# Optimization experiments

Measured on AMD Instinct MI355X. Metric: run time of the kernel, lower is better.

Reference implementation:

```python
import jax, jax.numpy as jnp
import numpy as np

N_NODES = 50000
N_EDGES = 800000
D = 128        # input_dim == output_dim
D_EDGE = 64    # edge_attr_size
Z_DIM = 2 * D + D_EDGE  # 320


def setup_inputs() -> dict:
    key = jax.random.key(0)
    k1, k2, k3, k4, k5 = jax.random.split(key, 5)
    x = jax.random.normal(k1, (N_NODES, D), dtype=jnp.float32)
    edge_index = jax.random.randint(k2, (2, N_EDGES), 0, N_NODES, dtype=jnp.int64)
    edge_attr = jax.random.normal(k3, (N_EDGES, D_EDGE), dtype=jnp.float32)
    scale = 1.0 / np.sqrt(Z_DIM)
    W_f = jax.random.normal(k4, (Z_DIM, D), dtype=jnp.float32) * scale
    W_s = jax.random.normal(k5, (Z_DIM, D), dtype=jnp.float32) * scale
    b_f = jnp.zeros((D,), dtype=jnp.float32)
    b_s = jnp.zeros((D,), dtype=jnp.float32)
    return {"x": x, "edge_index": edge_index, "edge_attr": edge_attr,
            "W_f": W_f, "b_f": b_f, "W_s": W_s, "b_s": b_s}


def reference(x, edge_index, edge_attr, W_f, b_f, W_s, b_s):
    # Dropout(p=0.0) is identity in inference.
    src = edge_index[0]  # j (message source)
    dst = edge_index[1]  # i (message target)
    # z_e = [x_i, x_j, e_ij]  -> [E, 2D + D_edge]
    z = jnp.concatenate([x[dst], x[src], edge_attr], axis=-1)
    # CGConv message: sigmoid(lin_f(z)) * softplus(lin_s(z))
    msg = jax.nn.sigmoid(z @ W_f + b_f) * jax.nn.softplus(z @ W_s + b_s)
    # scatter-add aggregation + residual
    out = jax.ops.segment_sum(msg, dst, num_segments=x.shape[0]) + x
    # use_activation=True -> ReLU
    return jax.nn.relu(out)
```

## Files before the change

kernel.cpp:

```cpp
#include <hip/hip_runtime.h>
#include <hip/hip_bf16.h>

#define E_TOTAL   800000
#define NN        50000
#define DD        128
#define DE        64
#define ZDIM      320
#define MT        64
#define NTPB      4
#define NBS       196

typedef short bf16x8 __attribute__((ext_vector_type(8)));
typedef float f32x4  __attribute__((ext_vector_type(4)));

__device__ __forceinline__ unsigned short f2bf(float f) {
    union { float f; unsigned int u; } v; v.f = f;
    unsigned int u = v.u;
    return (unsigned short)((u + 0x7fffu + ((u >> 16) & 1u)) >> 16);
}

__device__ __forceinline__ float bf2f(unsigned short h) {
    union { unsigned u; float f; } v; v.u = ((unsigned)h) << 16; return v.f;
}

__device__ __forceinline__ unsigned pkbf2(float a, float b) {
    __hip_bfloat162 h = __float22bfloat162_rn(make_float2(a, b));
    unsigned u; __builtin_memcpy(&u, &h, 4); return u;
}

__device__ __forceinline__ uint2 pkbf4(float4 v) {
    uint2 r; r.x = pkbf2(v.x, v.y); r.y = pkbf2(v.z, v.w); return r;
}

__device__ __forceinline__ float fast_rcp(float x) {
#if __has_builtin(__builtin_amdgcn_rcpf)
    return __builtin_amdgcn_rcpf(x);
#else
    return 1.0f / x;
#endif
}

__device__ __forceinline__ void barrier_lgkm() {
    __builtin_amdgcn_sched_barrier(0);
    asm volatile("s_waitcnt lgkmcnt(0)" ::: "memory");
    __builtin_amdgcn_s_barrier();
    __builtin_amdgcn_sched_barrier(0);
}


__global__ void scan_part(const int* __restrict__ counts, int* __restrict__ partial) {
    __shared__ int red[256];
    int t = threadIdx.x, k = blockIdx.x * 256 + t;
    red[t] = (k < NN) ? counts[k] : 0;
    __syncthreads();
    for (int d = 128; d > 0; d >>= 1) {
        if (t < d) red[t] += red[t + d];
        __syncthreads();
    }
    if (t == 0) partial[blockIdx.x] = red[0];
}

__global__ void scan_top(int* __restrict__ partial) {
    __shared__ int s[256];
    int t = threadIdx.x;
    int v = (t < NBS) ? partial[t] : 0;
    s[t] = v; __syncthreads();
    for (int d = 1; d < 256; d <<= 1) {
        int a = (t >= d) ? s[t - d] : 0;
        __syncthreads();
        s[t] += a;
        __syncthreads();
    }
    if (t < NBS) partial[t] = s[t] - v;
}

__global__ void scan_final(const int* __restrict__ counts,
                           const int* __restrict__ partial,
                           int* __restrict__ cursor) {
    __shared__ int s[256];
    int t = threadIdx.x, k = blockIdx.x * 256 + t;
    int v = (k < NN) ? counts[k] : 0;
    s[t] = v; __syncthreads();
    for (int d = 1; d < 256; d <<= 1) {
        int a = (t >= d) ? s[t - d] : 0;
        __syncthreads();
        s[t] += a;
        __syncthreads();
    }
    if (k < NN) cursor[k] = partial[blockIdx.x] + s[t] - v;
}

__global__ void scan_final2(const int* __restrict__ counts,
                            const int* __restrict__ partial,
                            int* __restrict__ cursor) {
    __shared__ int s[256], p2[256], orig[256];
    int t = threadIdx.x, k = blockIdx.x * 256 + t;
    int pv = (t < NBS) ? partial[t] : 0;
    p2[t] = pv; orig[t] = pv; __syncthreads();
    for (int d = 1; d < 256; d <<= 1) {
        int a = (t >= d) ? p2[t - d] : 0;
        __syncthreads();
        p2[t] += a;
        __syncthreads();
    }
    int blkoff = p2[blockIdx.x] - orig[blockIdx.x];
    int v = (k < NN) ? counts[k] : 0;
    s[t] = v; __syncthreads();
    for (int d = 1; d < 256; d <<= 1) {
        int a = (t >= d) ? s[t - d] : 0;
        __syncthreads();
        s[t] += a;
        __syncthreads();
    }
    if (k < NN) cursor[k] = blkoff + s[t] - v;
}

__global__ void scatter_kernel(const int* __restrict__ ei, int* __restrict__ cursor,
                               uint2* __restrict__ spak2) {
    int e = blockIdx.x * 256 + threadIdx.x;
    if (e < E_TOTAL) {
        int d = ei[E_TOTAL + e];
        int pos = atomicAdd(&cursor[d], 1);
        uint2 p; p.x = ((unsigned)d << 16) | (unsigned)ei[e]; p.y = (unsigned)e;
        spak2[pos] = p;
    }
}


__global__ void prep_kernel4(const int* __restrict__ ei,
                             const float* __restrict__ W_f,
                             const float* __restrict__ W_s,
                             unsigned short* __restrict__ WtE,
                             unsigned short* __restrict__ WtN,
                             int* __restrict__ counts,
                             float* __restrict__ aggr) {
    int id = blockIdx.x * 256 + threadIdx.x;
    float4 z; z.x = 0.f; z.y = 0.f; z.z = 0.f; z.w = 0.f;
    ((float4*)aggr)[id] = z;
    if (id < E_TOTAL) atomicAdd(&counts[ei[E_TOTAL + id]], 1);
    if (id < 256 * DE) {
        int n = id >> 6, k = id & 63;
        int ok = 2 * DD + k;
        float wv = (n < DD) ? W_f[ok * DD + n] : W_s[ok * DD + (n - DD)];
        WtE[id] = f2bf(wv);
    } else if (id < 256 * DE + 2 * 256 * DD) {
        int id2 = id - 256 * DE;
        int part = id2 >> 15;
        int r = id2 & 32767;
        int n = r >> 7, k = r & 127;
        int ok = part * DD + k;
        float wv = (n < DD) ? W_f[ok * DD + n] : W_s[ok * DD + (n - DD)];
        WtN[id2] = f2bf(wv);
    }
}

__global__ __launch_bounds__(512, 4)
void node_kernel3(const float* __restrict__ x,
                  const unsigned short* __restrict__ WtN,
                  const float* __restrict__ bf_, const float* __restrict__ bs_,
                  unsigned int* __restrict__ nodeP32) {
    __shared__ unsigned short A_lds[MT * DD];
    const int t = threadIdx.x;
    const int m_off = blockIdx.x * MT;
    const int lane = t & 63, w8 = t >> 6;
    const int part = w8 >> 2, w = w8 & 3;
    const int l15 = lane & 15, quad = lane >> 4;

    #pragma unroll
    for (int it = 0; it < 4; ++it) {
        int idx = it * 512 + t;
        int e = idx >> 5, kq = idx & 31;
        int row = m_off + e; if (row >= NN) row = NN - 1;
        float4 v = ((const float4*)(x + (size_t)row * DD))[kq];
        int g = kq >> 1;
        int col = ((g & ~7) | ((g & 7) ^ (e & 7))) * 8 + (kq & 1) * 4;
        *((uint2*)&A_lds[e * DD + col]) = pkbf4(v);
    }

    f32x4 acc[4][4] = {};
    const int nt0 = 2 * w;
    const unsigned short* Bp[4];
    #pragma unroll
    for (int u = 0; u < 4; ++u) {
        int nt = nt0 + ((u < 2) ? u : (6 + u));
        Bp[u] = WtN + (size_t)part * (256 * DD) +
                (size_t)(nt * 16 + l15) * DD + quad * 8;
    }
    __syncthreads();

    #pragma unroll
    for (int ks = 0; ks < 4; ++ks) {
        bf16x8 af[4], bfr[4];
        #pragma unroll
        for (int i = 0; i < 4; ++i) {
            int m = i * 16 + l15;
            int g = 4 * ks + quad;
            int col = ((g & ~7) | ((g & 7) ^ (l15 & 7))) * 8;
            af[i] = *((const bf16x8*)&A_lds[m * DD + col]);
        }
        #pragma unroll
        for (int u = 0; u < 4; ++u)
            bfr[u] = *((const bf16x8*)(Bp[u] + ks * 32));
        #pragma unroll
        for (int i = 0; i < 4; ++i)
            #pragma unroll
            for (int u = 0; u < 4; ++u)
                acc[i][u] = __builtin_amdgcn_mfma_f32_16x16x32_bf16(
                    af[i], bfr[u], acc[i][u], 0, 0, 0);
    }

    const int c0 = 32 * w + l15, c1 = c0 + 16;
    const float bf0 = part ? 0.f : bf_[c0], bs0 = part ? 0.f : bs_[c0];
    const float bf1 = part ? 0.f : bf_[c1], bs1 = part ? 0.f : bs_[c1];
    #pragma unroll
    for (int i = 0; i < 4; ++i)
        #pragma unroll
        for (int j = 0; j < 4; ++j) {
            int e = i * 16 + quad * 4 + j;
            int row = m_off + e;
            if (row < NN) {
                unsigned int* np = nodeP32 + (size_t)row * 256 + part * 128;
                np[c0] = pkbf2(acc[i][0][j] + bf0, acc[i][2][j] + bs0);
                np[c1] = pkbf2(acc[i][1][j] + bf1, acc[i][3][j] + bs1);
            }
        }
}


#define ISSUE_VA(VA, K)                                                        \
    _Pragma("unroll")                                                          \
    for (int it = 0; it < 2; ++it) {                                           \
        int idx = it * 512 + t;                                                \
        int e = idx >> 4;                                                      \
        VA[it] = ((const float4*)(ea + (size_t)eid_lds[K][e] * DE))[idx & 15]; \
    }

#define ISSUE_GATHER(PS, PD, K)                                                \
    _Pragma("unroll")                                                          \
    for (int i = 0; i < 4; ++i)                                                \
        _Pragma("unroll")                                                      \
        for (int j = 0; j < 4; ++j) {                                          \
            int e = i * 16 + quad * 4 + j;                                     \
            PS[i * 4 + j] = nodeP32[(size_t)src_lds[K][e] * 256 + 128 + c];    \
            PD[i * 4 + j] = nodeP32[(size_t)dst_lds[K][e] * 256 + c];          \
        }

#define STORE_A(VA, BUF)                                                       \
    _Pragma("unroll")                                                          \
    for (int it = 0; it < 2; ++it) {                                           \
        int idx = it * 512 + t;                                                \
        int e = idx >> 4, kq = idx & 15;                                       \
        int colx = (((kq >> 1) & 7) ^ (e & 7)) * 8 + (kq & 1) * 4;             \
        *((uint2*)&A_lds[BUF][e * DE + colx]) = pkbf4(VA[it]);                 \
    }

#define ZERO_ACC                                                               \
    { f32x4 zz = {};                                                           \
      _Pragma("unroll")                                                        \
      for (int i = 0; i < 4; ++i) { acc[i][0] = zz; acc[i][1] = zz; } }

#define GEMM_T(BUF)                                                            \
    _Pragma("unroll")                                                          \
    for (int ks = 0; ks < 2; ++ks) {                                           \
        bf16x8 af[4];                                                          \
        _Pragma("unroll")                                                      \
        for (int i = 0; i < 4; ++i) {                                          \
            int m = i * 16 + l15;                                              \
            int g = 4 * ks + quad;                                             \
            int colx = ((g & 7) ^ (l15 & 7)) * 8;                              \
            af[i] = *((const bf16x8*)&A_lds[BUF][m * DE + colx]);              \
        }                                                                      \
        _Pragma("unroll")                                                      \
        for (int i = 0; i < 4; ++i) {                                          \
            acc[i][0] = __builtin_amdgcn_mfma_f32_16x16x32_bf16(               \
                af[i], bfr[0][ks], acc[i][0], 0, 0, 0);                        \
            acc[i][1] = __builtin_amdgcn_mfma_f32_16x16x32_bf16(               \
                af[i], bfr[1][ks], acc[i][1], 0, 0, 0);                        \
        }                                                                      \
    }

#define EPILOG(PS, PD, K)                                                      \
    {                                                                          \
        int rprev = -1; float s0 = 0.f, nf = 0.f, ns = 0.f;                    \
        _Pragma("unroll")                                                      \
        for (int i = 0; i < 4; ++i)                                            \
            _Pragma("unroll")                                                  \
            for (int j = 0; j < 4; ++j) {                                      \
                int e = i * 16 + quad * 4 + j;                                 \
                int rid = runid_lds[K][e];                                     \
                if (rid != rprev) {                                            \
                    if (rprev >= 0) atomicAdd(&sumb[rprev][c], s0);            \
                    rprev = rid; s0 = 0.f;                                     \
                    unsigned pk = PD[i * 4 + j];                               \
                    nf = bf2f((unsigned short)(pk & 0xffffu));                 \
                    ns = bf2f((unsigned short)(pk >> 16));                     \
                }                                                              \
                unsigned pp = PS[i * 4 + j];                                   \
                float f  = acc[i][0][j] + nf + bf2f((unsigned short)(pp & 0xffffu)); \
                float sg = acc[i][1][j] + ns + bf2f((unsigned short)(pp >> 16));     \
                s0 += fast_rcp(1.f + __expf(-f)) *                             \
                      (fmaxf(sg, 0.f) + __logf(1.f + __expf(-fabsf(sg))));     \
            }                                                                  \
        atomicAdd(&sumb[rprev][c], s0);                                        \
    }

#define WRITEOUT(K)                                                            \
    {                                                                          \
        int ndk = nd_lds[K];                                                   \
        int col = t & 127, rb = t >> 7;                                        \
        for (int r = rb; r < ndk; r += 4) {                                    \
            float v = sumb[r][col];                                            \
            sumb[r][col] = 0.f;                                                \
            float* op = aggr + (size_t)rdst_lds[K][r] * DD + col;              \
            if (rbound_lds[K][r]) atomicAdd(op, v);                            \
            else *op = v;                                                      \
        }                                                                      \
    }

__global__ __launch_bounds__(512, 3)
void edge_kernel4(const float* __restrict__ ea,
                  const unsigned short* __restrict__ WtE,
                  const unsigned int* __restrict__ nodeP32,
                  float* __restrict__ aggr,
                  const uint2* __restrict__ spak2) {
    __shared__ float sumb[MT][DD];
    __shared__ alignas(16) unsigned short A_lds[2][MT * DE];
    __shared__ int dst_lds[NTPB][MT];
    __shared__ int src_lds[NTPB][MT];
    __shared__ int eid_lds[NTPB][MT];
    __shared__ int runid_lds[NTPB][MT];
    __shared__ int rdst_lds[NTPB][MT];
    __shared__ int rbound_lds[NTPB][MT];
    __shared__ int nd_lds[NTPB];

    const int t = threadIdx.x;
    const int blk_e0 = blockIdx.x * (MT * NTPB);
    const int lane = t & 63, w2 = t >> 6, l15 = lane & 15, quad = lane >> 4;
    const int c = 16 * w2 + l15;

    bf16x8 bfr[2][2];
    #pragma unroll
    for (int u = 0; u < 2; ++u) {
        int nt = w2 + u * 8;
        const unsigned short* bp = WtE + (size_t)(nt * 16 + l15) * DE + quad * 8;
        bfr[u][0] = *((const bf16x8*)bp);
        bfr[u][1] = *((const bf16x8*)(bp + 32));
    }

    if (w2 < NTPB) {
        int tb = blk_e0 + w2 * MT;
        uint2 p = spak2[tb + lane];
        int dsv = (int)(p.x >> 16);
        dst_lds[w2][lane] = dsv;
        src_lds[w2][lane] = (int)(p.x & 0xffffu);
        eid_lds[w2][lane] = (int)p.y;
        int updsv = __shfl_up(dsv, 1);
        int flag = (lane == 0 || dsv != updsv) ? 1 : 0;
        unsigned long long m = __ballot(flag != 0);
        int rid = __popcll(m << (63 - lane)) - 1;
        runid_lds[w2][lane] = rid;
        if (flag) { rdst_lds[w2][rid] = dsv; rbound_lds[w2][rid] = 0; }
        int ndv = __popcll(m);
        if (lane == 0) {
            nd_lds[w2] = ndv;
            if (tb > 0 && (int)(spak2[tb - 1].x >> 16) == dsv)
                rbound_lds[w2][0] = 1;
        }
        if (lane == MT - 1) {
            if (tb + MT < E_TOTAL && (int)(spak2[tb + MT].x >> 16) == dsv)
                rbound_lds[w2][ndv - 1] = 1;
        }
    }
    {
        int col = t & 127, rb = t >> 7;
        #pragma unroll
        for (int r = rb; r < MT; r += 4) sumb[r][col] = 0.f;
    }
    __syncthreads();

    float4 vaA[2], vaB[2];
    unsigned psA[16], psB[16], pdA[16], pdB[16];
    f32x4 acc[4][2];

    ISSUE_VA(vaA, 0)
    ISSUE_GATHER(psA, pdA, 0)
    STORE_A(vaA, 0)
    ISSUE_VA(vaB, 1)
    ISSUE_GATHER(psB, pdB, 1)
    barrier_lgkm();

    ZERO_ACC GEMM_T(0)
    EPILOG(psA, pdA, 0)
    ISSUE_VA(vaA, 2)
    ISSUE_GATHER(psA, pdA, 2)
    STORE_A(vaB, 1)
    barrier_lgkm();
    WRITEOUT(0)
    barrier_lgkm();

    ZERO_ACC GEMM_T(1)
    EPILOG(psB, pdB, 1)
    ISSUE_VA(vaB, 3)
    ISSUE_GATHER(psB, pdB, 3)
    STORE_A(vaA, 0)
    barrier_lgkm();
    WRITEOUT(1)
    barrier_lgkm();

    ZERO_ACC GEMM_T(0)
    EPILOG(psA, pdA, 2)
    STORE_A(vaB, 1)
    barrier_lgkm();
    WRITEOUT(2)
    barrier_lgkm();

    ZERO_ACC GEMM_T(1)
    EPILOG(psB, pdB, 3)
    barrier_lgkm();
    WRITEOUT(3)
}

__global__ void relu_kernel4(const float* __restrict__ x,
                             const float* __restrict__ aggr,
                             float* __restrict__ out) {
    int id = blockIdx.x * 256 + threadIdx.x;
    if (id < NN * DD / 4) {
        float4 xv = ((const float4*)x)[id];
        float4 av = ((const float4*)aggr)[id];
        float4 v;
        v.x = fmaxf(xv.x + av.x, 0.0f); v.y = fmaxf(xv.y + av.y, 0.0f);
        v.z = fmaxf(xv.z + av.z, 0.0f); v.w = fmaxf(xv.w + av.w, 0.0f);
        ((float4*)out)[id] = v;
    }
}


__global__ void prep_kernel2(const float* __restrict__ x,
                             const int* __restrict__ ei,
                             const float* __restrict__ W_f,
                             const float* __restrict__ W_s,
                             unsigned short* __restrict__ WtE,
                             unsigned short* __restrict__ WtN,
                             int* __restrict__ counts,
                             float* __restrict__ out) {
    int id = blockIdx.x * 256 + threadIdx.x;
    ((float4*)out)[id] = ((const float4*)x)[id];
    if (id < E_TOTAL) atomicAdd(&counts[ei[E_TOTAL + id]], 1);
    if (id < 256 * DE) {
        int n = id >> 6, k = id & 63;
        int ok = 2 * DD + k;
        float wv = (n < DD) ? W_f[ok * DD + n] : W_s[ok * DD + (n - DD)];
        WtE[id] = f2bf(wv);
    } else if (id < 256 * DE + 2 * 256 * DD) {
        int id2 = id - 256 * DE;
        int part = id2 >> 15;
        int r = id2 & 32767;
        int n = r >> 7, k = r & 127;
        int ok = part * DD + k;
        float wv = (n < DD) ? W_f[ok * DD + n] : W_s[ok * DD + (n - DD)];
        WtN[id2] = f2bf(wv);
    }
}

__global__ __launch_bounds__(256, 4)
void node_kernel2(const float* __restrict__ x,
                  const unsigned short* __restrict__ WtN,
                  const float* __restrict__ bf_, const float* __restrict__ bs_,
                  unsigned int* __restrict__ nodeP32) {
    __shared__ unsigned short A_lds[MT * DD];
    const int t = threadIdx.x;
    const int m_off = blockIdx.x * MT;
    const int part = blockIdx.y;
    const int lane = t & 63, w = t >> 6, l15 = lane & 15, quad = lane >> 4;

    #pragma unroll
    for (int it = 0; it < 8; ++it) {
        int idx = it * 256 + t;
        int e = idx >> 5, kq = idx & 31;
        int row = m_off + e; if (row >= NN) row = NN - 1;
        float4 v = ((const float4*)(x + (size_t)row * DD))[kq];
        int g = kq >> 1;
        int col = ((g & ~7) | ((g & 7) ^ (e & 7))) * 8 + (kq & 1) * 4;
        *((uint2*)&A_lds[e * DD + col]) = pkbf4(v);
    }

    f32x4 acc[4][4] = {};
    const int nt0 = 2 * w;
    const unsigned short* Bp[4];
    #pragma unroll
    for (int u = 0; u < 4; ++u) {
        int nt = nt0 + ((u < 2) ? u : (6 + u));
        Bp[u] = WtN + (size_t)part * (256 * DD) +
                (size_t)(nt * 16 + l15) * DD + quad * 8;
    }
    __syncthreads();

    #pragma unroll
    for (int ks = 0; ks < 4; ++ks) {
        bf16x8 af[4], bfr[4];
        #pragma unroll
        for (int i = 0; i < 4; ++i) {
            int m = i * 16 + l15;
            int g = 4 * ks + quad;
            int col = ((g & ~7) | ((g & 7) ^ (l15 & 7))) * 8;
            af[i] = *((const bf16x8*)&A_lds[m * DD + col]);
        }
        #pragma unroll
        for (int u = 0; u < 4; ++u)
            bfr[u] = *((const bf16x8*)(Bp[u] + ks * 32));
        #pragma unroll
        for (int i = 0; i < 4; ++i)
            #pragma unroll
            for (int u = 0; u < 4; ++u)
                acc[i][u] = __builtin_amdgcn_mfma_f32_16x16x32_bf16(
                    af[i], bfr[u], acc[i][u], 0, 0, 0);
    }

    const int c0 = 32 * w + l15, c1 = c0 + 16;
    const float bf0 = part ? 0.f : bf_[c0], bs0 = part ? 0.f : bs_[c0];
    const float bf1 = part ? 0.f : bf_[c1], bs1 = part ? 0.f : bs_[c1];
    #pragma unroll
    for (int i = 0; i < 4; ++i)
        #pragma unroll
        for (int j = 0; j < 4; ++j) {
            int e = i * 16 + quad * 4 + j;
            int row = m_off + e;
            if (row < NN) {
                unsigned int* np = nodeP32 + (size_t)row * 256 + part * 128;
                np[c0] = pkbf2(acc[i][0][j] + bf0, acc[i][2][j] + bs0);
                np[c1] = pkbf2(acc[i][1][j] + bf1, acc[i][3][j] + bs1);
            }
        }
}

__global__ __launch_bounds__(512, 4)
void edge_kernel2(const float* __restrict__ ea,
                  const unsigned short* __restrict__ WtE,
                  const unsigned int* __restrict__ nodeP32,
                  float* __restrict__ out,
                  const uint2* __restrict__ spak2) {
    __shared__ float sumb[MT][DD];
    __shared__ unsigned short A_lds[MT * DE];
    __shared__ int dst_lds[MT];
    __shared__ int src_lds[MT];
    __shared__ int eid_lds[MT];
    __shared__ int runid_lds[MT];
    __shared__ int rdst_lds[MT];
    __shared__ int rbound_lds[MT];
    __shared__ int ndist_lds;

    const int t = threadIdx.x;
    const int m_off = blockIdx.x * MT;
    const int lane = t & 63, w2 = t >> 6, l15 = lane & 15, quad = lane >> 4;

    if (t < MT) {
        uint2 p = spak2[m_off + t];
        int dsv = (int)(p.x >> 16);
        dst_lds[t] = dsv;
        src_lds[t] = (int)(p.x & 0xffffu);
        eid_lds[t] = (int)p.y;
        int updsv = __shfl_up(dsv, 1);
        int flag = (t == 0 || dsv != updsv) ? 1 : 0;
        unsigned long long m = __ballot(flag != 0);
        int rid = __popcll(m << (63 - t)) - 1;
        runid_lds[t] = rid;
        if (flag) { rdst_lds[rid] = dsv; rbound_lds[rid] = 0; }
        int nd = __popcll(m);
        if (t == 0) {
            ndist_lds = nd;
            if (m_off > 0 && (int)(spak2[m_off - 1].x >> 16) == dsv)
                rbound_lds[0] = 1;
        }
        if (t == MT - 1) {
            if (m_off + MT < E_TOTAL &&
                (int)(spak2[m_off + MT].x >> 16) == dsv)
                rbound_lds[nd - 1] = 1;
        }
    }
    __syncthreads();

    const int c = 16 * w2 + l15;

    float4 va[2];
    #pragma unroll
    for (int it = 0; it < 2; ++it) {
        int idx = it * 512 + t;
        int e = idx >> 4;
        va[it] = ((const float4*)(ea + (size_t)eid_lds[e] * DE))[idx & 15];
    }
    unsigned int ps[16], pd[16];
    #pragma unroll
    for (int i = 0; i < 4; ++i)
        #pragma unroll
        for (int j = 0; j < 4; ++j) {
            int e = i * 16 + quad * 4 + j;
            ps[i * 4 + j] = nodeP32[(size_t)src_lds[e] * 256 + 128 + c];
            pd[i * 4 + j] = nodeP32[(size_t)dst_lds[e] * 256 + c];
        }
    {
        int nd = ndist_lds;
        int col = t & 127, rb = t >> 7;
        for (int r = rb; r < nd; r += 4) sumb[r][col] = 0.f;
    }
    #pragma unroll
    for (int it = 0; it < 2; ++it) {
        int idx = it * 512 + t;
        int e = idx >> 4, kq = idx & 15;
        int g = kq >> 1;
        int col = ((g & 7) ^ (e & 7)) * 8 + (kq & 1) * 4;
        *((uint2*)&A_lds[e * DE + col]) = pkbf4(va[it]);
    }

    f32x4 acc[4][2] = {};
    const unsigned short* Bp[2];
    #pragma unroll
    for (int u = 0; u < 2; ++u) {
        int nt = w2 + u * 8;
        Bp[u] = WtE + (size_t)(nt * 16 + l15) * DE + quad * 8;
    }
    __syncthreads();

    #pragma unroll
    for (int ks = 0; ks < 2; ++ks) {
        bf16x8 af[4], bfr[2];
        #pragma unroll
        for (int i = 0; i < 4; ++i) {
            int m = i * 16 + l15;
            int g = 4 * ks + quad;
            int col = ((g & 7) ^ (l15 & 7)) * 8;
            af[i] = *((const bf16x8*)&A_lds[m * DE + col]);
        }
        #pragma unroll
        for (int u = 0; u < 2; ++u)
            bfr[u] = *((const bf16x8*)(Bp[u] + ks * 32));
        #pragma unroll
        for (int i = 0; i < 4; ++i)
            #pragma unroll
            for (int u = 0; u < 2; ++u)
                acc[i][u] = __builtin_amdgcn_mfma_f32_16x16x32_bf16(
                    af[i], bfr[u], acc[i][u], 0, 0, 0);
    }

    int rprev = -1;
    float s0 = 0.f, nf = 0.f, ns = 0.f;
    #pragma unroll
    for (int i = 0; i < 4; ++i)
        #pragma unroll
        for (int j = 0; j < 4; ++j) {
            int e = i * 16 + quad * 4 + j;
            int rid = runid_lds[e];
            if (rid != rprev) {
                if (rprev >= 0) atomicAdd(&sumb[rprev][c], s0);
                rprev = rid; s0 = 0.f;
                unsigned int pk = pd[i * 4 + j];
                nf = bf2f((unsigned short)(pk & 0xffffu));
                ns = bf2f((unsigned short)(pk >> 16));
            }
            unsigned int pp = ps[i * 4 + j];
            float f  = acc[i][0][j] + nf + bf2f((unsigned short)(pp & 0xffffu));
            float sg = acc[i][1][j] + ns + bf2f((unsigned short)(pp >> 16));
            s0 += fast_rcp(1.f + __expf(-f)) *
                  (fmaxf(sg, 0.f) + __logf(1.f + __expf(-fabsf(sg))));
        }
    atomicAdd(&sumb[rprev][c], s0);
    __syncthreads();

    {
        int nd = ndist_lds;
        int col = t & 127, rb = t >> 7;
        for (int r = rb; r < nd; r += 4) {
            float v = sumb[r][col];
            float* op = out + (size_t)rdst_lds[r] * DD + col;
            if (rbound_lds[r]) atomicAdd(op, v);
            else *op += v;
        }
    }
}

__global__ void relu_kernel(float* __restrict__ out) {
    int id = blockIdx.x * 256 + threadIdx.x;
    if (id < NN * DD / 4) {
        float4 v = ((float4*)out)[id];
        v.x = fmaxf(v.x, 0.0f); v.y = fmaxf(v.y, 0.0f);
        v.z = fmaxf(v.z, 0.0f); v.w = fmaxf(v.w, 0.0f);
        ((float4*)out)[id] = v;
    }
}


__global__ void prep_fb(const float* __restrict__ x,
                        const float* __restrict__ W_f,
                        const float* __restrict__ W_s,
                        unsigned short* __restrict__ Wt,
                        float* __restrict__ out) {
    int id = blockIdx.x * 256 + threadIdx.x;
    if (id < NN * DD / 4)
        ((float4*)out)[id] = ((const float4*)x)[id];
    if (id < 2 * DD * ZDIM) {
        int n = id / ZDIM, k = id - n * ZDIM;
        float wv = (n < DD) ? W_f[k * DD + n] : W_s[k * DD + (n - DD)];
        Wt[n * ZDIM + k] = f2bf(wv);
    }
}

__global__ __launch_bounds__(256, 3)
void edge_fb(const float* __restrict__ x,
             const int* __restrict__ ei,
             const float* __restrict__ ea,
             const unsigned short* __restrict__ Wt,
             const float* __restrict__ bf_,
             const float* __restrict__ bs_,
             float* __restrict__ out) {
    __shared__ unsigned short A_lds[MT * ZDIM];
    __shared__ int dst_lds[MT];
    __shared__ int src_lds[MT];

    const int t = threadIdx.x;
    const int m_off = blockIdx.x * MT;
    const int lane = t & 63, w = t >> 6, l15 = lane & 15, quad = lane >> 4;

    if (t < MT) dst_lds[t] = ei[E_TOTAL + m_off + t];
    else if (t < 2 * MT) src_lds[t - MT] = ei[m_off + (t - MT)];
    __syncthreads();

    #pragma unroll
    for (int it = 0; it < 4; ++it) {
        int idx = it * 256 + t;
        int e = idx >> 4, kq = idx & 15;
        float4 v = ((const float4*)(ea + (size_t)(m_off + e) * DE))[kq];
        int g = 32 + (kq >> 1);
        int col = ((g & ~7) | ((g & 7) ^ (e & 7))) * 8 + (kq & 1) * 4;
        *((uint2*)&A_lds[e * ZDIM + col]) = pkbf4(v);
    }
    #pragma unroll
    for (int it = 0; it < 8; ++it) {
        int idx = it * 256 + t;
        int e = idx >> 5, kq = idx & 31;
        float4 v = ((const float4*)(x + (size_t)dst_lds[e] * DD))[kq];
        int g = kq >> 1;
        int col = ((g & ~7) | ((g & 7) ^ (e & 7))) * 8 + (kq & 1) * 4;
        *((uint2*)&A_lds[e * ZDIM + col]) = pkbf4(v);
    }
    #pragma unroll
    for (int it = 0; it < 8; ++it) {
        int idx = it * 256 + t;
        int e = idx >> 5, kq = idx & 31;
        float4 v = ((const float4*)(x + (size_t)src_lds[e] * DD))[kq];
        int g = 16 + (kq >> 1);
        int col = ((g & ~7) | ((g & 7) ^ (e & 7))) * 8 + (kq & 1) * 4;
        *((uint2*)&A_lds[e * ZDIM + col]) = pkbf4(v);
    }

    f32x4 acc[4][4] = {};
    const int nt0 = 2 * w;
    const unsigned short* Bp[4];
    #pragma unroll
    for (int u = 0; u < 4; ++u) {
        int nt = nt0 + ((u < 2) ? u : (6 + u));
        Bp[u] = Wt + (size_t)(nt * 16 + l15) * ZDIM + quad * 8;
    }
    __syncthreads();

    #pragma unroll
    for (int ks = 0; ks < 10; ++ks) {
        bf16x8 af[4], bfr[4];
        #pragma unroll
        for (int i = 0; i < 4; ++i) {
            int m = i * 16 + l15;
            int g = 4 * ks + quad;
            int col = ((g & ~7) | ((g & 7) ^ (l15 & 7))) * 8;
            af[i] = *((const bf16x8*)&A_lds[m * ZDIM + col]);
        }
        #pragma unroll
        for (int u = 0; u < 4; ++u)
            bfr[u] = *((const bf16x8*)(Bp[u] + ks * 32));
        #pragma unroll
        for (int i = 0; i < 4; ++i)
            #pragma unroll
            for (int u = 0; u < 4; ++u)
                acc[i][u] = __builtin_amdgcn_mfma_f32_16x16x32_bf16(
                    af[i], bfr[u], acc[i][u], 0, 0, 0);
    }

    const int c0 = 32 * w + l15, c1 = c0 + 16;
    const float bf0 = bf_[c0], bs0 = bs_[c0], bf1 = bf_[c1], bs1 = bs_[c1];
    #pragma unroll
    for (int i = 0; i < 4; ++i)
        #pragma unroll
        for (int j = 0; j < 4; ++j) {
            int e = i * 16 + quad * 4 + j;
            float* op = out + (size_t)dst_lds[e] * DD;
            float f0 = acc[i][0][j] + bf0;
            float sg0 = acc[i][2][j] + bs0;
            atomicAdd(op + c0, fast_rcp(1.f + __expf(-f0)) *
                (fmaxf(sg0, 0.f) + __logf(1.f + __expf(-fabsf(sg0)))));
            float f1 = acc[i][1][j] + bf1;
            float sg1 = acc[i][3][j] + bs1;
            atomicAdd(op + c1, fast_rcp(1.f + __expf(-f1)) *
                (fmaxf(sg1, 0.f) + __logf(1.f + __expf(-fabsf(sg1)))));
        }
}


extern "C" void kernel_launch(void* const* d_in, const int* in_sizes, int n_in,
                              void* d_out, int out_size, void* d_ws, size_t ws_size,
                              hipStream_t stream) {
    (void)in_sizes; (void)n_in; (void)out_size;
    const float* x   = (const float*)d_in[0];
    const int*   ei  = (const int*)d_in[1];
    const float* ea  = (const float*)d_in[2];
    const float* W_f = (const float*)d_in[3];
    const float* b_f = (const float*)d_in[4];
    const float* W_s = (const float*)d_in[5];
    const float* b_s = (const float*)d_in[6];
    float* out = (float*)d_out;

    char* ws = (char*)d_ws;
    const size_t WS_NEED4 = 83764864;
    const size_t WS_NEED2 = 58164864;

    if (ws_size >= WS_NEED4) {
        unsigned short* WtE2   = (unsigned short*)ws;
        unsigned short* WtN2   = (unsigned short*)(ws + 32768);
        int*            counts = (int*)(ws + 163840);
        int*            cursor = (int*)(ws + 363840);
        int*            partial= (int*)(ws + 563840);
        uint2*          spak2  = (uint2*)(ws + 564864);
        unsigned int*   nodeP32= (unsigned int*)(ws + 6964864);
        float*          aggr   = (float*)(ws + 58164864);

        hipMemsetAsync(counts, 0, NN * sizeof(int), stream);
        prep_kernel4<<<NN * DD / 4 / 256, 256, 0, stream>>>(
            ei, W_f, W_s, WtE2, WtN2, counts, aggr);
        scan_part<<<NBS, 256, 0, stream>>>(counts, partial);
        scan_final2<<<NBS, 256, 0, stream>>>(counts, partial, cursor);
        scatter_kernel<<<(E_TOTAL + 255) / 256, 256, 0, stream>>>(ei, cursor, spak2);
        node_kernel3<<<(NN + MT - 1) / MT, 512, 0, stream>>>(
            x, WtN2, b_f, b_s, nodeP32);
        edge_kernel4<<<E_TOTAL / (MT * NTPB), 512, 0, stream>>>(
            ea, WtE2, nodeP32, aggr, spak2);
        relu_kernel4<<<6250, 256, 0, stream>>>(x, aggr, out);
    } else if (ws_size >= WS_NEED2) {
        unsigned short* WtE2   = (unsigned short*)ws;
        unsigned short* WtN2   = (unsigned short*)(ws + 32768);
        int*            counts = (int*)(ws + 163840);
        int*            cursor = (int*)(ws + 363840);
        int*            partial= (int*)(ws + 563840);
        uint2*          spak2  = (uint2*)(ws + 564864);
        unsigned int*   nodeP32= (unsigned int*)(ws + 6964864);

        hipMemsetAsync(counts, 0, NN * sizeof(int), stream);
        prep_kernel2<<<NN * DD / 4 / 256, 256, 0, stream>>>(
            x, ei, W_f, W_s, WtE2, WtN2, counts, out);
        scan_part<<<NBS, 256, 0, stream>>>(counts, partial);
        scan_top<<<1, 256, 0, stream>>>(partial);
        scan_final<<<NBS, 256, 0, stream>>>(counts, partial, cursor);
        scatter_kernel<<<(E_TOTAL + 255) / 256, 256, 0, stream>>>(ei, cursor, spak2);
        dim3 ng((NN + MT - 1) / MT, 2);
        node_kernel2<<<ng, 256, 0, stream>>>(x, WtN2, b_f, b_s, nodeP32);
        edge_kernel2<<<E_TOTAL / MT, 512, 0, stream>>>(
            ea, WtE2, nodeP32, out, spak2);
        relu_kernel<<<6250, 256, 0, stream>>>(out);
    } else {
        unsigned short* Wt = (unsigned short*)ws;
        prep_fb<<<6250, 256, 0, stream>>>(x, W_f, W_s, Wt, out);
        edge_fb<<<E_TOTAL / MT, 256, 0, stream>>>(x, ei, ea, Wt, b_f, b_s, out);
        relu_kernel<<<6250, 256, 0, stream>>>(out);
    }
}
```

Measured before the change: 706.1 us.

## Replace multi-tile software-pipelined edge kernel with one tile per block

The edge kernel no longer processes four 64-edge tiles per block with double-buffered LDS and prefetch of the next tile's gathers. Each block now handles a single tile, which uses less shared memory and allows four blocks per CU instead of three. The B fragments are loaded from global memory inside the k-loop rather than preloaded into registers, and only the used sumb rows are zeroed. The kernel now relies on occupancy rather than explicit intra-block prefetch to hide gather latency, at the cost of four times more blocks and repeated per-block setup.

After: 601.8 us. -14.8%, faster.

```diff
diff --git a/kernel.cpp b/kernel.cpp
--- a/kernel.cpp
+++ b/kernel.cpp
@@ -7,7 +7,6 @@
 #define DE        64
 #define ZDIM      320
 #define MT        64
-#define NTPB      4
 #define NBS       196
 
 typedef short bf16x8 __attribute__((ext_vector_type(8)));
@@ -38,13 +37,6 @@
 #else
     return 1.0f / x;
 #endif
-}
-
-__device__ __forceinline__ void barrier_lgkm() {
-    __builtin_amdgcn_sched_barrier(0);
-    asm volatile("s_waitcnt lgkmcnt(0)" ::: "memory");
-    __builtin_amdgcn_s_barrier();
-    __builtin_amdgcn_sched_barrier(0);
 }
 
 
@@ -226,198 +218,148 @@
         }
 }
 
-
-#define ISSUE_VA(VA, K)                                                        \
-    _Pragma("unroll")                                                          \
-    for (int it = 0; it < 2; ++it) {                                           \
-        int idx = it * 512 + t;                                                \
-        int e = idx >> 4;                                                      \
-        VA[it] = ((const float4*)(ea + (size_t)eid_lds[K][e] * DE))[idx & 15]; \
-    }
-
-#define ISSUE_GATHER(PS, PD, K)                                                \
-    _Pragma("unroll")                                                          \
-    for (int i = 0; i < 4; ++i)                                                \
-        _Pragma("unroll")                                                      \
-        for (int j = 0; j < 4; ++j) {                                          \
-            int e = i * 16 + quad * 4 + j;                                     \
-            PS[i * 4 + j] = nodeP32[(size_t)src_lds[K][e] * 256 + 128 + c];    \
-            PD[i * 4 + j] = nodeP32[(size_t)dst_lds[K][e] * 256 + c];          \
-        }
-
-#define STORE_A(VA, BUF)                                                       \
-    _Pragma("unroll")                                                          \
-    for (int it = 0; it < 2; ++it) {                                           \
-        int idx = it * 512 + t;                                                \
-        int e = idx >> 4, kq = idx & 15;                                       \
-        int colx = (((kq >> 1) & 7) ^ (e & 7)) * 8 + (kq & 1) * 4;             \
-        *((uint2*)&A_lds[BUF][e * DE + colx]) = pkbf4(VA[it]);                 \
-    }
-
-#define ZERO_ACC                                                               \
-    { f32x4 zz = {};                                                           \
-      _Pragma("unroll")                                                        \
-      for (int i = 0; i < 4; ++i) { acc[i][0] = zz; acc[i][1] = zz; } }
-
-#define GEMM_T(BUF)                                                            \
-    _Pragma("unroll")                                                          \
-    for (int ks = 0; ks < 2; ++ks) {                                           \
-        bf16x8 af[4];                                                          \
-        _Pragma("unroll")                                                      \
-        for (int i = 0; i < 4; ++i) {                                          \
-            int m = i * 16 + l15;                                              \
-            int g = 4 * ks + quad;                                             \
-            int colx = ((g & 7) ^ (l15 & 7)) * 8;                              \
-            af[i] = *((const bf16x8*)&A_lds[BUF][m * DE + colx]);              \
-        }                                                                      \
-        _Pragma("unroll")                                                      \
-        for (int i = 0; i < 4; ++i) {                                          \
-            acc[i][0] = __builtin_amdgcn_mfma_f32_16x16x32_bf16(               \
-                af[i], bfr[0][ks], acc[i][0], 0, 0, 0);                        \
-            acc[i][1] = __builtin_amdgcn_mfma_f32_16x16x32_bf16(               \
-                af[i], bfr[1][ks], acc[i][1], 0, 0, 0);                        \
-        }                                                                      \
-    }
-
-#define EPILOG(PS, PD, K)                                                      \
-    {                                                                          \
-        int rprev = -1; float s0 = 0.f, nf = 0.f, ns = 0.f;                    \
-        _Pragma("unroll")                                                      \
-        for (int i = 0; i < 4; ++i)                                            \
-            _Pragma("unroll")                                                  \
-            for (int j = 0; j < 4; ++j) {                                      \
-                int e = i * 16 + quad * 4 + j;                                 \
-                int rid = runid_lds[K][e];                                     \
-                if (rid != rprev) {                                            \
-                    if (rprev >= 0) atomicAdd(&sumb[rprev][c], s0);            \
-                    rprev = rid; s0 = 0.f;                                     \
-                    unsigned pk = PD[i * 4 + j];                               \
-                    nf = bf2f((unsigned short)(pk & 0xffffu));                 \
-                    ns = bf2f((unsigned short)(pk >> 16));                     \
-                }                                                              \
-                unsigned pp = PS[i * 4 + j];                                   \
-                float f  = acc[i][0][j] + nf + bf2f((unsigned short)(pp & 0xffffu)); \
-                float sg = acc[i][1][j] + ns + bf2f((unsigned short)(pp >> 16));     \
-                s0 += fast_rcp(1.f + __expf(-f)) *                             \
-                      (fmaxf(sg, 0.f) + __logf(1.f + __expf(-fabsf(sg))));     \
-            }                                                                  \
-        atomicAdd(&sumb[rprev][c], s0);                                        \
-    }
-
-#define WRITEOUT(K)                                                            \
-    {                                                                          \
-        int ndk = nd_lds[K];                                                   \
-        int col = t & 127, rb = t >> 7;                                        \
-        for (int r = rb; r < ndk; r += 4) {                                    \
-            float v = sumb[r][col];                                            \
-            sumb[r][col] = 0.f;                                                \
-            float* op = aggr + (size_t)rdst_lds[K][r] * DD + col;              \
-            if (rbound_lds[K][r]) atomicAdd(op, v);                            \
-            else *op = v;                                                      \
-        }                                                                      \
-    }
-
-__global__ __launch_bounds__(512, 3)
-void edge_kernel4(const float* __restrict__ ea,
+__global__ __launch_bounds__(512, 4)
+void edge_kernel5(const float* __restrict__ ea,
                   const unsigned short* __restrict__ WtE,
                   const unsigned int* __restrict__ nodeP32,
                   float* __restrict__ aggr,
                   const uint2* __restrict__ spak2) {
     __shared__ float sumb[MT][DD];
-    __shared__ alignas(16) unsigned short A_lds[2][MT * DE];
-    __shared__ int dst_lds[NTPB][MT];
-    __shared__ int src_lds[NTPB][MT];
-    __shared__ int eid_lds[NTPB][MT];
-    __shared__ int runid_lds[NTPB][MT];
-    __shared__ int rdst_lds[NTPB][MT];
-    __shared__ int rbound_lds[NTPB][MT];
-    __shared__ int nd_lds[NTPB];
+    __shared__ unsigned short A_lds[MT * DE];
+    __shared__ int dst_lds[MT];
+    __shared__ int src_lds[MT];
+    __shared__ int eid_lds[MT];
+    __shared__ int runid_lds[MT];
+    __shared__ int rdst_lds[MT];
+    __shared__ int rbound_lds[MT];
+    __shared__ int ndist_lds;
 
     const int t = threadIdx.x;
-    const int blk_e0 = blockIdx.x * (MT * NTPB);
+    const int m_off = blockIdx.x * MT;
     const int lane = t & 63, w2 = t >> 6, l15 = lane & 15, quad = lane >> 4;
+
+    if (t < MT) {
+        uint2 p = spak2[m_off + t];
+        int dsv = (int)(p.x >> 16);
+        dst_lds[t] = dsv;
+        src_lds[t] = (int)(p.x & 0xffffu);
+        eid_lds[t] = (int)p.y;
+        int updsv = __shfl_up(dsv, 1);
+        int flag = (t == 0 || dsv != updsv) ? 1 : 0;
+        unsigned long long m = __ballot(flag != 0);
+        int rid = __popcll(m << (63 - t)) - 1;
+        runid_lds[t] = rid;
+        if (flag) { rdst_lds[rid] = dsv; rbound_lds[rid] = 0; }
+        int nd = __popcll(m);
+        if (t == 0) {
+            ndist_lds = nd;
+            if (m_off > 0 && (int)(spak2[m_off - 1].x >> 16) == dsv)
+                rbound_lds[0] = 1;
+        }
+        if (t == MT - 1) {
+            if (m_off + MT < E_TOTAL &&
+                (int)(spak2[m_off + MT].x >> 16) == dsv)
+                rbound_lds[nd - 1] = 1;
+        }
+    }
+    __syncthreads();
+
     const int c = 16 * w2 + l15;
 
-    bf16x8 bfr[2][2];
+    float4 va[2];
+    #pragma unroll
+    for (int it = 0; it < 2; ++it) {
+        int idx = it * 512 + t;
+        int e = idx >> 4;
+        va[it] = ((const float4*)(ea + (size_t)eid_lds[e] * DE))[idx & 15];
+    }
+    unsigned int ps[16], pd[16];
+    #pragma unroll
+    for (int i = 0; i < 4; ++i)
+        #pragma unroll
+        for (int j = 0; j < 4; ++j) {
+            int e = i * 16 + quad * 4 + j;
+            ps[i * 4 + j] = nodeP32[(size_t)src_lds[e] * 256 + 128 + c];
+            pd[i * 4 + j] = nodeP32[(size_t)dst_lds[e] * 256 + c];
+        }
+    {
+        int nd = ndist_lds;
+        int col = t & 127, rb = t >> 7;
+        for (int r = rb; r < nd; r += 4) sumb[r][col] = 0.f;
+    }
+    #pragma unroll
+    for (int it = 0; it < 2; ++it) {
+        int idx = it * 512 + t;
+        int e = idx >> 4, kq = idx & 15;
+        int g = kq >> 1;
+        int col = ((g & 7) ^ (e & 7)) * 8 + (kq & 1) * 4;
+        *((uint2*)&A_lds[e * DE + col]) = pkbf4(va[it]);
+    }
+
+    f32x4 acc[4][2] = {};
+    const unsigned short* Bp[2];
     #pragma unroll
     for (int u = 0; u < 2; ++u) {
         int nt = w2 + u * 8;
-        const unsigned short* bp = WtE + (size_t)(nt * 16 + l15) * DE + quad * 8;
-        bfr[u][0] = *((const bf16x8*)bp);
-        bfr[u][1] = *((const bf16x8*)(bp + 32));
-    }
-
-    if (w2 < NTPB) {
-        int tb = blk_e0 + w2 * MT;
-        uint2 p = spak2[tb + lane];
-        int dsv = (int)(p.x >> 16);
-        dst_lds[w2][lane] = dsv;
-        src_lds[w2][lane] = (int)(p.x & 0xffffu);
-        eid_lds[w2][lane] = (int)p.y;
-        int updsv = __shfl_up(dsv, 1);
-        int flag = (lane == 0 || dsv != updsv) ? 1 : 0;
-        unsigned long long m = __ballot(flag != 0);
-        int rid = __popcll(m << (63 - lane)) - 1;
-        runid_lds[w2][lane] = rid;
-        if (flag) { rdst_lds[w2][rid] = dsv; rbound_lds[w2][rid] = 0; }
-        int ndv = __popcll(m);
-        if (lane == 0) {
-            nd_lds[w2] = ndv;
-            if (tb > 0 && (int)(spak2[tb - 1].x >> 16) == dsv)
-                rbound_lds[w2][0] = 1;
-        }
-        if (lane == MT - 1) {
-            if (tb + MT < E_TOTAL && (int)(spak2[tb + MT].x >> 16) == dsv)
-                rbound_lds[w2][ndv - 1] = 1;
-        }
-    }
+        Bp[u] = WtE + (size_t)(nt * 16 + l15) * DE + quad * 8;
+    }
+    __syncthreads();
+
+    #pragma unroll
+    for (int ks = 0; ks < 2; ++ks) {
+        bf16x8 af[4], bfr[2];
+        #pragma unroll
+        for (int i = 0; i < 4; ++i) {
+            int m = i * 16 + l15;
+            int g = 4 * ks + quad;
+            int col = ((g & 7) ^ (l15 & 7)) * 8;
+            af[i] = *((const bf16x8*)&A_lds[m * DE + col]);
+        }
+        #pragma unroll
+        for (int u = 0; u < 2; ++u)
+            bfr[u] = *((const bf16x8*)(Bp[u] + ks * 32));
+        #pragma unroll
+        for (int i = 0; i < 4; ++i)
+            #pragma unroll
+            for (int u = 0; u < 2; ++u)
+                acc[i][u] = __builtin_amdgcn_mfma_f32_16x16x32_bf16(
+                    af[i], bfr[u], acc[i][u], 0, 0, 0);
+    }
+
+    int rprev = -1;
+    float s0 = 0.f, nf = 0.f, ns = 0.f;
+    #pragma unroll
+    for (int i = 0; i < 4; ++i)
+        #pragma unroll
+        for (int j = 0; j < 4; ++j) {
+            int e = i * 16 + quad * 4 + j;
+            int rid = runid_lds[e];
+            if (rid != rprev) {
+                if (rprev >= 0) atomicAdd(&sumb[rprev][c], s0);
+                rprev = rid; s0 = 0.f;
+                unsigned int pk = pd[i * 4 + j];
+                nf = bf2f((unsigned short)(pk & 0xffffu));
+                ns = bf2f((unsigned short)(pk >> 16));
+            }
+            unsigned int pp = ps[i * 4 + j];
+            float f  = acc[i][0][j] + nf + bf2f((unsigned short)(pp & 0xffffu));
+            float sg = acc[i][1][j] + ns + bf2f((unsigned short)(pp >> 16));
+            s0 += fast_rcp(1.f + __expf(-f)) *
+                  (fmaxf(sg, 0.f) + __logf(1.f + __expf(-fabsf(sg))));
+        }
+    atomicAdd(&sumb[rprev][c], s0);
+    __syncthreads();
+
     {
+        int nd = ndist_lds;
         int col = t & 127, rb = t >> 7;
-        #pragma unroll
-        for (int r = rb; r < MT; r += 4) sumb[r][col] = 0.f;
-    }
-    __syncthreads();
-
-    float4 vaA[2], vaB[2];
-    unsigned psA[16], psB[16], pdA[16], pdB[16];
-    f32x4 acc[4][2];
-
-    ISSUE_VA(vaA, 0)
-    ISSUE_GATHER(psA, pdA, 0)
-    STORE_A(vaA, 0)
-    ISSUE_VA(vaB, 1)
-    ISSUE_GATHER(psB, pdB, 1)
-    barrier_lgkm();
-
-    ZERO_ACC GEMM_T(0)
-    EPILOG(psA, pdA, 0)
-    ISSUE_VA(vaA, 2)
-    ISSUE_GATHER(psA, pdA, 2)
-    STORE_A(vaB, 1)
-    barrier_lgkm();
-    WRITEOUT(0)
-    barrier_lgkm();
-
-    ZERO_ACC GEMM_T(1)
-    EPILOG(psB, pdB, 1)
-    ISSUE_VA(vaB, 3)
-    ISSUE_GATHER(psB, pdB, 3)
-    STORE_A(vaA, 0)
-    barrier_lgkm();
-    WRITEOUT(1)
-    barrier_lgkm();
-
-    ZERO_ACC GEMM_T(0)
-    EPILOG(psA, pdA, 2)
-    STORE_A(vaB, 1)
-    barrier_lgkm();
-    WRITEOUT(2)
-    barrier_lgkm();
-
-    ZERO_ACC GEMM_T(1)
-    EPILOG(psB, pdB, 3)
-    barrier_lgkm();
-    WRITEOUT(3)
+        for (int r = rb; r < nd; r += 4) {
+            float v = sumb[r][col];
+            float* op = aggr + (size_t)rdst_lds[r] * DD + col;
+            if (rbound_lds[r]) atomicAdd(op, v);
+            else *op = v;
+        }
+    }
 }
 
 __global__ void relu_kernel4(const float* __restrict__ x,
@@ -837,7 +779,7 @@
         scatter_kernel<<<(E_TOTAL + 255) / 256, 256, 0, stream>>>(ei, cursor, spak2);
         node_kernel3<<<(NN + MT - 1) / MT, 512, 0, stream>>>(
             x, WtN2, b_f, b_s, nodeP32);
-        edge_kernel4<<<E_TOTAL / (MT * NTPB), 512, 0, stream>>>(
+        edge_kernel5<<<E_TOTAL / MT, 512, 0, stream>>>(
             ea, WtE2, nodeP32, aggr, spak2);
         relu_kernel4<<<6250, 256, 0, stream>>>(x, aggr, out);
     } else if (ws_size >= WS_NEED2) {
```
